# Optimization experiments

Hardware: AMD Instinct MI355X
Metric: run time of the kernel (lower is better)

Reference implementation:

```python
import jax, jax.numpy as jnp
import numpy as np

N, D = 32768, 512          # rows, input dim (row count 32-aligned per source)
C, K = 16, 16              # ncodebooks, codewords per codebook (4-bit codes)
S = D // C                 # subvector length per codebook
M = 1024                   # output columns (W_test.shape[1])


def setup_inputs() -> dict:
    key = jax.random.key(0)
    k1, k2, k3 = jax.random.split(key, 3)
    X = jax.random.normal(k1, (N, D), dtype=jnp.float32)
    protos = jax.random.normal(k2, (C, K, S), dtype=jnp.float32)
    luts = jax.random.normal(k3, (C, K, M), dtype=jnp.float32)
    return {"X": X, "protos": protos, "luts": luts}


def reference(X, protos, luts):
    n, d = X.shape
    c, k, s = protos.shape
    # --- PQ encode: nearest prototype per codebook subvector ---
    Xr = X.reshape(n, c, s)                                   # [N, C, S]
    dots = jnp.einsum("ncs,cks->nck", Xr, protos)             # [N, C, K]
    dists = (protos * protos).sum(-1)[None, :, :] - 2.0 * dots
    codes = jnp.argmin(dists, axis=-1)                        # [N, C] int codes
    # --- LUT gather-accumulate: out[n,m] = sum_c luts[c, codes[n,c], m] ---
    onehot = jax.nn.one_hot(codes, k, dtype=luts.dtype)       # [N, C, K]
    out = jnp.einsum("nck,ckm->nm", onehot, luts)             # [N, M]
    # forward() scales the approximate product by mean(X)
    return out * jnp.mean(X)
```

## Files before the change

kernel.cpp:

```cpp
#include <hip/hip_runtime.h>
#include <hip/hip_bf16.h>
#include <stdint.h>
#include <string.h>

#define N_ROWS 32768
#define DIM    512
#define CB     16
#define KW     16
#define SV     32
#define MCOLS  1024

typedef __attribute__((ext_vector_type(8))) short bf16x8_t;
typedef __attribute__((ext_vector_type(4))) float f32x4_t;


__global__ __launch_bounds__(256) void prep_kernel(
    const float* __restrict__ protos, double* __restrict__ protos_d,
    double* __restrict__ norms_d)
{
    const int tid  = threadIdx.x;
    const int c    = blockIdx.x;
    const int base = c * (KW * SV);
    protos_d[base + tid]       = (double)protos[base + tid];
    protos_d[base + tid + 256] = (double)protos[base + tid + 256];
    if (tid < KW) {
        const float* src = protos + base + tid * SV;
        double nk = 0.0;
        #pragma unroll
        for (int j = 0; j < SV; ++j) { double v = (double)src[j]; nk += v * v; }
        norms_d[c * KW + tid] = nk;
    }
}

__global__ __launch_bounds__(256, 4) void encode_kernel(
    const float* __restrict__ X, const double* __restrict__ protos_d,
    const double* __restrict__ norms_d, uint8_t* __restrict__ codes,
    double* __restrict__ sum_out)
{
    __shared__ __align__(16) float xs[256 * 32];
    __shared__ double redsum[4];

    const int tid  = threadIdx.x;
    const int lane = tid & 63;
    const int wv   = tid >> 6;
    const int c    = blockIdx.x & 15;
    const int n0   = (blockIdx.x >> 4) * 256;

    double sx = 0.0;
    {
        const int ch = tid & 7;
        const int rr = tid >> 3;
        #pragma unroll
        for (int it = 0; it < 8; ++it) {
            const int row = it * 32 + rr;
            const float4 v = *(const float4*)(X + (size_t)(n0 + row) * DIM
                                              + c * SV + ch * 4);
            *(float4*)&xs[row * 32 + ((ch ^ (row & 7)) << 2)] = v;
            sx += (double)v.x + (double)v.y + (double)v.z + (double)v.w;
        }
    }
    __syncthreads();

    double xd[SV];
    #pragma unroll
    for (int j = 0; j < 8; ++j) {
        const float4 v = *(const float4*)&xs[tid * 32 + ((j ^ (tid & 7)) << 2)];
        xd[j * 4 + 0] = (double)v.x; xd[j * 4 + 1] = (double)v.y;
        xd[j * 4 + 2] = (double)v.z; xd[j * 4 + 3] = (double)v.w;
    }

    const double* __restrict__ Pd = protos_d + (size_t)c * (KW * SV);
    const double* __restrict__ Nd = norms_d + (size_t)c * KW;

    double best = 1e300;
    int bk = 0;
    #pragma unroll
    for (int k = 0; k < KW; ++k) {
        const double* pk = Pd + k * SV;
        double d0 = 0.0, d1 = 0.0, d2 = 0.0, d3 = 0.0;
        #pragma unroll
        for (int s = 0; s < 8; ++s) {
            d0 += xd[4 * s + 0] * pk[4 * s + 0];
            d1 += xd[4 * s + 1] * pk[4 * s + 1];
            d2 += xd[4 * s + 2] * pk[4 * s + 2];
            d3 += xd[4 * s + 3] * pk[4 * s + 3];
        }
        double dist = Nd[k] - 2.0 * ((d0 + d1) + (d2 + d3));
        if (dist < best) { best = dist; bk = k; }
    }
    codes[(size_t)(n0 + tid) * CB + c] = (uint8_t)bk;

    #pragma unroll
    for (int off = 32; off > 0; off >>= 1) sx += __shfl_down(sx, off);
    if (lane == 0) redsum[wv] = sx;
    __syncthreads();
    if (tid == 0) {
        double s = redsum[0] + redsum[1] + redsum[2] + redsum[3];
        atomicAdd(sum_out, s);
    }
}

__global__ __launch_bounds__(256, 4) void lut_mfma_kernel(
    const float* __restrict__ luts, const uint8_t* __restrict__ codes,
    const double* __restrict__ sum_in, float* __restrict__ out)
{
    __shared__ __align__(16) uint16_t lut_s[64 * 256];

    const int tid   = threadIdx.x;
    const int mtile = blockIdx.x & 15;
    const int nblk  = blockIdx.x >> 4;
    const int m0 = mtile * 64;
    const int n0 = nblk * 512;

    const float scale = (float)(sum_in[0] * (1.0 / ((double)N_ROWS * (double)DIM)));

    for (int i = tid; i < 256 * 64; i += 256) {
        const int ck = i >> 6, m = i & 63;
        float v = luts[(size_t)ck * MCOLS + m0 + m] * scale;
        __hip_bfloat16 b = __float2bfloat16(v);
        lut_s[m * 256 + (ck ^ ((m & 7) << 3))] = *(const uint16_t*)&b;
    }
    __syncthreads();

    const int wv   = tid >> 6;
    const int lane = tid & 63;
    const int mloc = lane & 15;
    const int half = lane >> 4;
    const int sel  = half & 1;
    const int h2   = half >> 1;
    const int shiftbase = h2 * 8;
    const int sel8 = sel * 8;
    const int swz  = (mloc & 7) << 3;

    #pragma unroll
    for (int rtq = 0; rtq < 2; ++rtq) {
        const int rowbase = wv * 128 + rtq * 64;

        uint4 crow[4];
        #pragma unroll
        for (int rt = 0; rt < 4; ++rt)
            crow[rt] = *(const uint4*)(codes
                         + (size_t)(n0 + rowbase + rt * 16 + mloc) * CB);

        f32x4_t acc[4][4];
        #pragma unroll
        for (int rt = 0; rt < 4; ++rt)
            #pragma unroll
            for (int ct = 0; ct < 4; ++ct)
                acc[rt][ct] = (f32x4_t){0.f, 0.f, 0.f, 0.f};

        #pragma unroll
        for (int ki = 0; ki < 8; ++ki) {
            bf16x8_t bf[4];
            const int kidx = (ki * 32 + half * 8) ^ swz;
            #pragma unroll
            for (int ct = 0; ct < 4; ++ct) {
                const uint16_t* bp = lut_s + (ct * 16 + mloc) * 256 + kidx;
                bf[ct] = *reinterpret_cast<const bf16x8_t*>(bp);
            }
            #pragma unroll
            for (int rt = 0; rt < 4; ++rt) {
                const uint32_t cws[4] = {crow[rt].x, crow[rt].y,
                                         crow[rt].z, crow[rt].w};
                const uint32_t code =
                    (cws[ki >> 1] >> (shiftbase + (ki & 1) * 16)) & 0xffu;
                const int t = (int)code - sel8;
                const uint64_t sh = 0x3F80ull << ((t & 3) * 16);
                const int q = t >> 2;
                union { uint64_t u[2]; bf16x8_t v8; } A;
                A.u[0] = (q == 0) ? sh : 0ull;
                A.u[1] = (q == 1) ? sh : 0ull;
                #pragma unroll
                for (int ct = 0; ct < 4; ++ct)
                    acc[rt][ct] = __builtin_amdgcn_mfma_f32_16x16x32_bf16(
                        bf[ct], A.v8, acc[rt][ct], 0, 0, 0);
            }
        }

        #pragma unroll
        for (int rt = 0; rt < 4; ++rt) {
            const int grow = n0 + rowbase + rt * 16 + mloc;
            float* rowp = out + (size_t)grow * MCOLS + m0 + half * 4;
            #pragma unroll
            for (int ct = 0; ct < 4; ++ct)
                *reinterpret_cast<f32x4_t*>(rowp + ct * 16) = acc[rt][ct];
        }
    }
}

extern "C" void kernel_launch(void* const* d_in, const int* in_sizes, int n_in,
                              void* d_out, int out_size, void* d_ws, size_t ws_size,
                              hipStream_t stream) {
    const float* X      = (const float*)d_in[0];
    const float* protos = (const float*)d_in[1];
    const float* luts   = (const float*)d_in[2];
    float* out = (float*)d_out;

    double*  sum_ws   = (double*)d_ws;
    double*  protos_d = (double*)((uint8_t*)d_ws + 256);
    double*  norms_d  = (double*)((uint8_t*)d_ws + 66048);
    uint8_t* codes    = (uint8_t*)d_ws + 68352;

    hipMemsetAsync(d_ws, 0, 8, stream);

    prep_kernel<<<dim3(16), dim3(256), 0, stream>>>(protos, protos_d, norms_d);

    encode_kernel<<<dim3(2048), dim3(256), 0, stream>>>(X, protos_d, norms_d,
                                                        codes, sum_ws);

    lut_mfma_kernel<<<dim3(1024), dim3(256), 0, stream>>>(luts, codes, sum_ws, out);
}
```

Baseline: 231.1 us.

## Fold prototype prep into encode kernel and spread mean atomics across slots

Drops the separate prep kernel that converted prototypes to double and computed norms. The encode kernel now reads float prototypes directly, converting them in registers, and computes the per-codebook norms into shared memory. The single global atomic for the X sum is split into 16 per-codebook slots spaced 64 bytes apart, which the LUT kernel adds up. This removes a kernel launch and reduces atomic contention, at the cost of redundant norm computation in every block and extra float-to-double conversions in the hot loop.

```diff
diff --git a/kernel.cpp b/kernel.cpp
--- a/kernel.cpp
+++ b/kernel.cpp
@@ -14,30 +14,12 @@
 typedef __attribute__((ext_vector_type(4))) float f32x4_t;
 
 
-__global__ __launch_bounds__(256) void prep_kernel(
-    const float* __restrict__ protos, double* __restrict__ protos_d,
-    double* __restrict__ norms_d)
-{
-    const int tid  = threadIdx.x;
-    const int c    = blockIdx.x;
-    const int base = c * (KW * SV);
-    protos_d[base + tid]       = (double)protos[base + tid];
-    protos_d[base + tid + 256] = (double)protos[base + tid + 256];
-    if (tid < KW) {
-        const float* src = protos + base + tid * SV;
-        double nk = 0.0;
-        #pragma unroll
-        for (int j = 0; j < SV; ++j) { double v = (double)src[j]; nk += v * v; }
-        norms_d[c * KW + tid] = nk;
-    }
-}
-
 __global__ __launch_bounds__(256, 4) void encode_kernel(
-    const float* __restrict__ X, const double* __restrict__ protos_d,
-    const double* __restrict__ norms_d, uint8_t* __restrict__ codes,
-    double* __restrict__ sum_out)
+    const float* __restrict__ X, const float* __restrict__ protos,
+    uint8_t* __restrict__ codes, double* __restrict__ sum_ws)
 {
     __shared__ __align__(16) float xs[256 * 32];
+    __shared__ double nd_s[KW];
     __shared__ double redsum[4];
 
     const int tid  = threadIdx.x;
@@ -45,6 +27,16 @@
     const int wv   = tid >> 6;
     const int c    = blockIdx.x & 15;
     const int n0   = (blockIdx.x >> 4) * 256;
+
+    const float* __restrict__ pf = protos + c * (KW * SV);
+
+    if (tid < KW) {
+        const float* src = pf + tid * SV;
+        double nk = 0.0;
+        #pragma unroll
+        for (int j = 0; j < SV; ++j) { double v = (double)src[j]; nk += v * v; }
+        nd_s[tid] = nk;
+    }
 
     double sx = 0.0;
     {
@@ -69,23 +61,20 @@
         xd[j * 4 + 2] = (double)v.z; xd[j * 4 + 3] = (double)v.w;
     }
 
-    const double* __restrict__ Pd = protos_d + (size_t)c * (KW * SV);
-    const double* __restrict__ Nd = norms_d + (size_t)c * KW;
-
     double best = 1e300;
     int bk = 0;
     #pragma unroll
     for (int k = 0; k < KW; ++k) {
-        const double* pk = Pd + k * SV;
+        const float* pk = pf + k * SV;
         double d0 = 0.0, d1 = 0.0, d2 = 0.0, d3 = 0.0;
         #pragma unroll
         for (int s = 0; s < 8; ++s) {
-            d0 += xd[4 * s + 0] * pk[4 * s + 0];
-            d1 += xd[4 * s + 1] * pk[4 * s + 1];
-            d2 += xd[4 * s + 2] * pk[4 * s + 2];
-            d3 += xd[4 * s + 3] * pk[4 * s + 3];
+            d0 += xd[4 * s + 0] * (double)pk[4 * s + 0];
+            d1 += xd[4 * s + 1] * (double)pk[4 * s + 1];
+            d2 += xd[4 * s + 2] * (double)pk[4 * s + 2];
+            d3 += xd[4 * s + 3] * (double)pk[4 * s + 3];
         }
-        double dist = Nd[k] - 2.0 * ((d0 + d1) + (d2 + d3));
+        double dist = nd_s[k] - 2.0 * ((d0 + d1) + (d2 + d3));
         if (dist < best) { best = dist; bk = k; }
     }
     codes[(size_t)(n0 + tid) * CB + c] = (uint8_t)bk;
@@ -96,7 +85,7 @@
     __syncthreads();
     if (tid == 0) {
         double s = redsum[0] + redsum[1] + redsum[2] + redsum[3];
-        atomicAdd(sum_out, s);
+        atomicAdd(&sum_ws[c * 8], s);
     }
 }
 
@@ -112,7 +101,10 @@
     const int m0 = mtile * 64;
     const int n0 = nblk * 512;
 
-    const float scale = (float)(sum_in[0] * (1.0 / ((double)N_ROWS * (double)DIM)));
+    double ssum = 0.0;
+    #pragma unroll
+    for (int i = 0; i < CB; ++i) ssum += sum_in[i * 8];
+    const float scale = (float)(ssum * (1.0 / ((double)N_ROWS * (double)DIM)));
 
     for (int i = tid; i < 256 * 64; i += 256) {
         const int ck = i >> 6, m = i & 63;
@@ -126,10 +118,8 @@
     const int lane = tid & 63;
     const int mloc = lane & 15;
     const int half = lane >> 4;
-    const int sel  = half & 1;
-    const int h2   = half >> 1;
-    const int shiftbase = h2 * 8;
-    const int sel8 = sel * 8;
+    const int sel8 = (half & 1) * 8;
+    const int shiftbase = (half >> 1) * 8;
     const int swz  = (mloc & 7) << 3;
 
     #pragma unroll
@@ -196,17 +186,12 @@
     const float* luts   = (const float*)d_in[2];
     float* out = (float*)d_out;
 
-    double*  sum_ws   = (double*)d_ws;
-    double*  protos_d = (double*)((uint8_t*)d_ws + 256);
-    double*  norms_d  = (double*)((uint8_t*)d_ws + 66048);
-    uint8_t* codes    = (uint8_t*)d_ws + 68352;
+    double*  sum_ws = (double*)d_ws;
+    uint8_t* codes  = (uint8_t*)d_ws + 1024;
 
-    hipMemsetAsync(d_ws, 0, 8, stream);
+    hipMemsetAsync(d_ws, 0, 1024, stream);
 
-    prep_kernel<<<dim3(16), dim3(256), 0, stream>>>(protos, protos_d, norms_d);
-
-    encode_kernel<<<dim3(2048), dim3(256), 0, stream>>>(X, protos_d, norms_d,
-                                                        codes, sum_ws);
+    encode_kernel<<<dim3(2048), dim3(256), 0, stream>>>(X, protos, codes, sum_ws);
 
     lut_mfma_kernel<<<dim3(1024), dim3(256), 0, stream>>>(luts, codes, sum_ws, out);
 }
```

After: 215.3 us. 1.07x faster.
